# Optimization experiments

Hardware: AMD Instinct MI355X
Metric: run time of the kernel (lower is better)

The kernel has to match this reference:

```python
import jax, jax.numpy as jnp
import numpy as np

N = 100000      # nodes
E = 1600000     # edges (avg degree 16)
D = 64          # in_channels == conv widths == lin width
G = 64          # graphs in batch
OUT = 10        # out_channels


def setup_inputs() -> dict:
    key = jax.random.key(0)
    ks = jax.random.split(key, 20)
    s = 0.1
    inp = {
        "x": jax.random.normal(ks[0], (N, D), jnp.float32),
        "edge_index": jax.random.randint(ks[1], (2, E), 0, N, dtype=jnp.int64),
        "batch": jnp.sort(jax.random.randint(ks[2], (N,), 0, G, dtype=jnp.int64)),
    }
    k = 3
    for i in range(3):  # 3 SAGEConv layers: lin_l (Wl, bl) on aggregated, lin_r (Wr, no bias) on root
        inp[f"c{i}_Wl"] = jax.random.normal(ks[k], (D, D), jnp.float32) * s; k += 1
        inp[f"c{i}_bl"] = jnp.zeros((D,), jnp.float32)
        inp[f"c{i}_Wr"] = jax.random.normal(ks[k], (D, D), jnp.float32) * s; k += 1
    inp["l0_W"] = jax.random.normal(ks[k], (D, D), jnp.float32) * s; k += 1
    inp["l0_b"] = jnp.zeros((D,), jnp.float32)
    inp["out_W"] = jax.random.normal(ks[k], (D, OUT), jnp.float32) * s; k += 1
    inp["out_b"] = jnp.zeros((OUT,), jnp.float32)
    return inp


def reference(x, edge_index, batch,
              c0_Wl, c0_bl, c0_Wr,
              c1_Wl, c1_bl, c1_Wr,
              c2_Wl, c2_bl, c2_Wr,
              l0_W, l0_b, out_W, out_b):
    src, dst = edge_index[0], edge_index[1]
    # in-degree of each target node (mean conv aggregation), computed once
    deg = jax.ops.segment_sum(jnp.ones((E,), x.dtype), dst, num_segments=N)
    inv_deg = (1.0 / jnp.maximum(deg, 1.0))[:, None]

    def sage(h, Wl, bl, Wr):
        # gather source features, mean-aggregate at targets, then lin_l(agg) + lin_r(h)
        agg = jax.ops.segment_sum(h[src], dst, num_segments=N) * inv_deg
        return agg @ Wl + bl + h @ Wr

    h = jax.nn.relu(sage(x, c0_Wl, c0_bl, c0_Wr))
    h = jax.nn.relu(sage(h, c1_Wl, c1_bl, c1_Wr))
    h = jax.nn.relu(sage(h, c2_Wl, c2_bl, c2_Wr))

    # global mean pool over graphs
    cnt = jax.ops.segment_sum(jnp.ones((N,), h.dtype), batch, num_segments=G)
    g = jax.ops.segment_sum(h, batch, num_segments=G) / jnp.maximum(cnt, 1.0)[:, None]

    g = jax.nn.relu(g @ l0_W + l0_b)
    return g @ out_W + out_b  # [G, OUT]
```

## Files before the change

kernel.cpp:

```cpp
#include <hip/hip_runtime.h>
#include <hip/hip_fp16.h>

#define WPB 8
#define PADK 136
#define BSH 8
#define BNODES 256
#define SC_BLOCKS 256
#define HIST_BLOCKS 256
#define HSTRIDE 512

typedef _Float16 half8 __attribute__((ext_vector_type(8)));
typedef float floatx4 __attribute__((ext_vector_type(4)));

#define TS16(v) (((((v)[0] + (v)[1]) + ((v)[2] + (v)[3])) + (((v)[4] + (v)[5]) + ((v)[6] + (v)[7]))) + \
                 ((((v)[8] + (v)[9]) + ((v)[10] + (v)[11])) + (((v)[12] + (v)[13]) + ((v)[14] + (v)[15]))))

__global__ __launch_bounds__(256) void gnn_pre(const int* __restrict__ dst,
                                               int* __restrict__ bkt_cnt, int nbkt, int E,
                                               const int* __restrict__ batch,
                                               float* __restrict__ gcnt, int N,
                                               const float4* __restrict__ xin,
                                               ushort4* __restrict__ x16o, int n4,
                                               __half* __restrict__ x16,
                                               __half* __restrict__ hA,
                                               __half* __restrict__ hB,
                                               int* __restrict__ hist_all) {
    int tid = threadIdx.x;
    if (blockIdx.x < HIST_BLOCKS) {
        __shared__ int h[512];
        __shared__ int gb[64];
        for (int i = tid; i < nbkt; i += 256) h[i] = 0;
        if (tid < 64) gb[tid] = 0;
        __syncthreads();
        const int stride = HIST_BLOCKS * 256;
        for (int e = blockIdx.x * 256 + tid; e < E; e += stride)
            atomicAdd(&h[dst[e] >> BSH], 1);
        for (int i = blockIdx.x * 256 + tid; i < N; i += stride)
            atomicAdd(&gb[batch[i]], 1);
        __syncthreads();
        for (int i = tid; i < nbkt; i += 256) {
            int v = h[i];
            hist_all[blockIdx.x * HSTRIDE + i] = v;
            if (v) atomicAdd(&bkt_cnt[i], v);
        }
        if (tid < 64) {
            int v = gb[tid];
            if (v) atomicAdd(&gcnt[tid], (float)v);
        }
        if (blockIdx.x == 0 && tid < 64) {
            x16[(size_t)N * 64 + tid] = __ushort_as_half((unsigned short)0);
            hA[(size_t)N * 64 + tid] = __ushort_as_half((unsigned short)0);
            hB[(size_t)N * 64 + tid] = __ushort_as_half((unsigned short)0);
        }
    } else {
        int i = (blockIdx.x - HIST_BLOCKS) * 256 + tid;
        if (i < n4) {
            float4 f = xin[i];
            ushort4 o;
            o.x = __half_as_ushort(__float2half(f.x));
            o.y = __half_as_ushort(__float2half(f.y));
            o.z = __half_as_ushort(__float2half(f.z));
            o.w = __half_as_ushort(__float2half(f.w));
            x16o[i] = o;
        }
    }
}

__global__ void gnn_bkt_scan(const int* __restrict__ bkt_cnt, int* __restrict__ bkt_base,
                             int* __restrict__ row_ptr, int nbkt, int N) {
    int lane = threadIdx.x;
    int carry = 0;
    for (int base = 0; base < nbkt; base += 64) {
        int idx = base + lane;
        int v = (idx < nbkt) ? bkt_cnt[idx] : 0;
        int x = v;
#pragma unroll
        for (int off = 1; off < 64; off <<= 1) {
            int y = __shfl_up(x, off);
            if (lane >= off) x += y;
        }
        if (idx < nbkt) bkt_base[idx] = carry + (x - v);
        carry += __shfl(x, 63);
    }
    if (lane == 0) {
        bkt_base[nbkt] = carry;
        row_ptr[N] = carry;
    }
}

__global__ __launch_bounds__(256) void gnn_scan2(const int* __restrict__ hist_all,
                                                 const int* __restrict__ bkt_base,
                                                 int* __restrict__ blk_base_all, int nbkt) {
    int b = blockIdx.x;
    int t = threadIdx.x, lane = t & 63, wv = t >> 6;
    __shared__ int wsum[4];
    int v = hist_all[t * HSTRIDE + b];
    int x = v;
#pragma unroll
    for (int off = 1; off < 64; off <<= 1) {
        int y = __shfl_up(x, off);
        if (lane >= off) x += y;
    }
    if (lane == 63) wsum[wv] = x;
    __syncthreads();
    int wexcl = 0;
    for (int w = 0; w < wv; w++) wexcl += wsum[w];
    blk_base_all[t * HSTRIDE + b] = bkt_base[b] + wexcl + (x - v);
}

__global__ __launch_bounds__(256) void gnn_bkt_scatter(const int* __restrict__ src,
                                                       const int* __restrict__ dst,
                                                       const int* __restrict__ blk_base_all,
                                                       unsigned int* __restrict__ pairs,
                                                       int E, int nbkt) {
    __shared__ int cur[512];
    int tid = threadIdx.x;
    for (int i = tid; i < nbkt; i += 256) cur[i] = blk_base_all[blockIdx.x * HSTRIDE + i];
    __syncthreads();
    const int stride = SC_BLOCKS * 256;
    for (int e = blockIdx.x * 256 + tid; e < E; e += stride) {
        int d = dst[e];
        int b = d >> BSH;
        int p = atomicAdd(&cur[b], 1);
        pairs[p] = (unsigned int)src[e] | ((unsigned int)(d & (BNODES - 1)) << 24);
    }
}

__global__ __launch_bounds__(256) void gnn_bkt_csr(const unsigned int* __restrict__ pairs,
                                                   const int* __restrict__ bkt_base,
                                                   int* __restrict__ row_ptr,
                                                   float* __restrict__ inv_deg,
                                                   int* __restrict__ csr_src, int N) {
    __shared__ int hist[BNODES];
    __shared__ int excl[BNODES];
    __shared__ int cur[BNODES];
    int b = blockIdx.x;
    int base = bkt_base[b];
    int cnt = bkt_base[b + 1] - base;
    int nd0 = b << BSH;
    int tid = threadIdx.x;
    hist[tid] = 0;
    __syncthreads();
    for (int i = tid; i < cnt; i += 256) atomicAdd(&hist[pairs[base + i] >> 24], 1);
    __syncthreads();
    if (tid < 64) {
        int carry = 0;
#pragma unroll
        for (int c = 0; c < BNODES; c += 64) {
            int v = hist[c + tid];
            int x = v;
#pragma unroll
            for (int off = 1; off < 64; off <<= 1) {
                int y = __shfl_up(x, off);
                if (tid >= off) x += y;
            }
            excl[c + tid] = carry + (x - v);
            carry += __shfl(x, 63);
        }
    }
    __syncthreads();
    {
        int node = nd0 + tid;
        if (node < N) {
            row_ptr[node] = base + excl[tid];
            int d = hist[tid];
            inv_deg[node] = 1.0f / (float)(d > 1 ? d : 1);
        }
        cur[tid] = excl[tid];
    }
    __syncthreads();
    for (int i = tid; i < cnt; i += 256) {
        unsigned int u = pairs[base + i];
        int j = u >> 24;
        int pos = atomicAdd(&cur[j], 1);
        csr_src[base + pos] = (int)(u & 0xFFFFFFu);
    }
}

__global__ __launch_bounds__(512, 6) void gnn_sage(const __half* __restrict__ hin,
                                                   __half* __restrict__ hout,
                                                   const int* __restrict__ row_ptr,
                                                   const int* __restrict__ csr_src,
                                                   const float* __restrict__ inv_deg,
                                                   const float* __restrict__ Wl,
                                                   const float* __restrict__ bl,
                                                   const float* __restrict__ Wr, int n) {
    __shared__ _Float16 w_lds[64 * PADK];
    __shared__ _Float16 in_lds[WPB][16 * PADK];
    int tid = threadIdx.x, lane = tid & 63, wv = tid >> 6;
    for (int i = tid; i < 64 * 64; i += 512) {
        int k = i >> 6, nn = i & 63;
        w_lds[nn * PADK + k] = (_Float16)Wl[i];
        w_lds[nn * PADK + 64 + k] = (_Float16)Wr[i];
    }
    __syncthreads();
    int ngroups = (n + 15) >> 4;
    int g = blockIdx.x * WPB + wv;
    if (g >= ngroups) return;
    int m16 = lane & 15, quad = lane >> 4;
    float bias[4];
#pragma unroll
    for (int nt = 0; nt < 4; nt++) bias[nt] = bl[nt * 16 + m16];
    _Float16* my_in = in_lds[wv];
    const _Float16* hin16 = (const _Float16*)hin;
    int nd0 = g << 4;
    for (int j2 = 0; j2 < 16; j2 += 2) {
        int ndA = min(nd0 + j2, n - 1);
        int ndB = min(nd0 + j2 + 1, n - 1);
        int s0A = row_ptr[ndA], s1A = row_ptr[ndA + 1];
        int s0B = row_ptr[ndB], s1B = row_ptr[ndB + 1];
        float idgA = inv_deg[ndA], idgB = inv_deg[ndB];
        my_in[j2 * PADK + 64 + lane] = hin16[(size_t)ndA * 64 + lane];
        my_in[(j2 + 1) * PADK + 64 + lane] = hin16[(size_t)ndB * 64 + lane];
        float accA = 0.0f, accB = 0.0f;
        int cbA = min(64, s1A - s0A);
        int cbB = min(64, s1B - s0B);
        int eA = (lane < cbA) ? csr_src[s0A + lane] : n;
        int eB = (lane < cbB) ? csr_src[s0B + lane] : n;
#pragma unroll
        for (int ib = 0; ib < 4; ib++) {
            const int i0 = ib * 16;
            if (i0 < cbA) {
                float vA[16];
#pragma unroll
                for (int j = 0; j < 16; j++) {
                    int sj = __shfl(eA, i0 + j);
                    vA[j] = __half2float(hin[(size_t)sj * 64 + lane]);
                }
                accA += TS16(vA);
            }
            if (i0 < cbB) {
                float vB[16];
#pragma unroll
                for (int j = 0; j < 16; j++) {
                    int sj = __shfl(eB, i0 + j);
                    vB[j] = __half2float(hin[(size_t)sj * 64 + lane]);
                }
                accB += TS16(vB);
            }
        }
        for (int base = s0A + 64; base < s1A; base += 64) {
            int cb = min(64, s1A - base);
            int ei = (lane < cb) ? csr_src[base + lane] : n;
#pragma unroll
            for (int ib = 0; ib < 4; ib++) {
                const int i0 = ib * 16;
                if (i0 < cb) {
                    float v[16];
#pragma unroll
                    for (int j = 0; j < 16; j++) {
                        int s = __shfl(ei, i0 + j);
                        v[j] = __half2float(hin[(size_t)s * 64 + lane]);
                    }
                    accA += TS16(v);
                }
            }
        }
        for (int base = s0B + 64; base < s1B; base += 64) {
            int cb = min(64, s1B - base);
            int ei = (lane < cb) ? csr_src[base + lane] : n;
#pragma unroll
            for (int ib = 0; ib < 4; ib++) {
                const int i0 = ib * 16;
                if (i0 < cb) {
                    float v[16];
#pragma unroll
                    for (int j = 0; j < 16; j++) {
                        int s = __shfl(ei, i0 + j);
                        v[j] = __half2float(hin[(size_t)s * 64 + lane]);
                    }
                    accB += TS16(v);
                }
            }
        }
        my_in[j2 * PADK + lane] = (_Float16)(accA * idgA);
        my_in[(j2 + 1) * PADK + lane] = (_Float16)(accB * idgB);
    }
    half8 afrag[4];
    const _Float16* abase = my_in + m16 * PADK + quad * 8;
#pragma unroll
    for (int ks = 0; ks < 4; ks++) afrag[ks] = *(const half8*)(abase + ks * 32);
    floatx4 accv[4];
#pragma unroll
    for (int nt = 0; nt < 4; nt++) {
        accv[nt].x = 0.f; accv[nt].y = 0.f; accv[nt].z = 0.f; accv[nt].w = 0.f;
    }
#pragma unroll
    for (int nt = 0; nt < 4; nt++) {
        const _Float16* bbase = w_lds + (nt * 16 + m16) * PADK + quad * 8;
#pragma unroll
        for (int ks = 0; ks < 4; ks++) {
            half8 bfrag = *(const half8*)(bbase + ks * 32);
            accv[nt] = __builtin_amdgcn_mfma_f32_16x16x32_f16(afrag[ks], bfrag, accv[nt], 0, 0, 0);
        }
    }
#pragma unroll
    for (int nt = 0; nt < 4; nt++) {
#pragma unroll
        for (int r = 0; r < 4; r++) {
            int node = nd0 + quad * 4 + r;
            if (node < n) {
                float v = fmaxf(accv[nt][r] + bias[nt], 0.0f);
                hout[(size_t)node * 64 + nt * 16 + m16] = __float2half(v);
            }
        }
    }
}

__global__ __launch_bounds__(512, 6) void gnn_sage_pool(const __half* __restrict__ hin,
                                                        const int* __restrict__ row_ptr,
                                                        const int* __restrict__ csr_src,
                                                        const float* __restrict__ inv_deg,
                                                        const float* __restrict__ Wl,
                                                        const float* __restrict__ bl,
                                                        const float* __restrict__ Wr,
                                                        const int* __restrict__ batch,
                                                        float* __restrict__ gsum, int n) {
    __shared__ _Float16 w_lds[64 * PADK];
    __shared__ _Float16 in_lds[WPB][16 * PADK];
    int tid = threadIdx.x, lane = tid & 63, wv = tid >> 6;
    for (int i = tid; i < 64 * 64; i += 512) {
        int k = i >> 6, nn = i & 63;
        w_lds[nn * PADK + k] = (_Float16)Wl[i];
        w_lds[nn * PADK + 64 + k] = (_Float16)Wr[i];
    }
    __syncthreads();
    int ngroups = (n + 15) >> 4;
    int g = blockIdx.x * WPB + wv;
    if (g >= ngroups) return;
    int m16 = lane & 15, quad = lane >> 4;
    float bias[4];
#pragma unroll
    for (int nt = 0; nt < 4; nt++) bias[nt] = bl[nt * 16 + m16];
    _Float16* my_in = in_lds[wv];
    const _Float16* hin16 = (const _Float16*)hin;
    int nd0 = g << 4;
    for (int j2 = 0; j2 < 16; j2 += 2) {
        int ndA = min(nd0 + j2, n - 1);
        int ndB = min(nd0 + j2 + 1, n - 1);
        int s0A = row_ptr[ndA], s1A = row_ptr[ndA + 1];
        int s0B = row_ptr[ndB], s1B = row_ptr[ndB + 1];
        float idgA = inv_deg[ndA], idgB = inv_deg[ndB];
        my_in[j2 * PADK + 64 + lane] = hin16[(size_t)ndA * 64 + lane];
        my_in[(j2 + 1) * PADK + 64 + lane] = hin16[(size_t)ndB * 64 + lane];
        float accA = 0.0f, accB = 0.0f;
        int cbA = min(64, s1A - s0A);
        int cbB = min(64, s1B - s0B);
        int eA = (lane < cbA) ? csr_src[s0A + lane] : n;
        int eB = (lane < cbB) ? csr_src[s0B + lane] : n;
#pragma unroll
        for (int ib = 0; ib < 4; ib++) {
            const int i0 = ib * 16;
            if (i0 < cbA) {
                float vA[16];
#pragma unroll
                for (int j = 0; j < 16; j++) {
                    int sj = __shfl(eA, i0 + j);
                    vA[j] = __half2float(hin[(size_t)sj * 64 + lane]);
                }
                accA += TS16(vA);
            }
            if (i0 < cbB) {
                float vB[16];
#pragma unroll
                for (int j = 0; j < 16; j++) {
                    int sj = __shfl(eB, i0 + j);
                    vB[j] = __half2float(hin[(size_t)sj * 64 + lane]);
                }
                accB += TS16(vB);
            }
        }
        for (int base = s0A + 64; base < s1A; base += 64) {
            int cb = min(64, s1A - base);
            int ei = (lane < cb) ? csr_src[base + lane] : n;
#pragma unroll
            for (int ib = 0; ib < 4; ib++) {
                const int i0 = ib * 16;
                if (i0 < cb) {
                    float v[16];
#pragma unroll
                    for (int j = 0; j < 16; j++) {
                        int s = __shfl(ei, i0 + j);
                        v[j] = __half2float(hin[(size_t)s * 64 + lane]);
                    }
                    accA += TS16(v);
                }
            }
        }
        for (int base = s0B + 64; base < s1B; base += 64) {
            int cb = min(64, s1B - base);
            int ei = (lane < cb) ? csr_src[base + lane] : n;
#pragma unroll
            for (int ib = 0; ib < 4; ib++) {
                const int i0 = ib * 16;
                if (i0 < cb) {
                    float v[16];
#pragma unroll
                    for (int j = 0; j < 16; j++) {
                        int s = __shfl(ei, i0 + j);
                        v[j] = __half2float(hin[(size_t)s * 64 + lane]);
                    }
                    accB += TS16(v);
                }
            }
        }
        my_in[j2 * PADK + lane] = (_Float16)(accA * idgA);
        my_in[(j2 + 1) * PADK + lane] = (_Float16)(accB * idgB);
    }
    half8 afrag[4];
    const _Float16* abase = my_in + m16 * PADK + quad * 8;
#pragma unroll
    for (int ks = 0; ks < 4; ks++) afrag[ks] = *(const half8*)(abase + ks * 32);
    floatx4 accv[4];
#pragma unroll
    for (int nt = 0; nt < 4; nt++) {
        accv[nt].x = 0.f; accv[nt].y = 0.f; accv[nt].z = 0.f; accv[nt].w = 0.f;
    }
#pragma unroll
    for (int nt = 0; nt < 4; nt++) {
        const _Float16* bbase = w_lds + (nt * 16 + m16) * PADK + quad * 8;
#pragma unroll
        for (int ks = 0; ks < 4; ks++) {
            half8 bfrag = *(const half8*)(bbase + ks * 32);
            accv[nt] = __builtin_amdgcn_mfma_f32_16x16x32_f16(afrag[ks], bfrag, accv[nt], 0, 0, 0);
        }
    }
    int bFirst = batch[nd0];
    int bLast = batch[min(nd0 + 15, n - 1)];
    if (bFirst == bLast && nd0 + 15 < n) {
#pragma unroll
        for (int nt = 0; nt < 4; nt++) {
            float s = fmaxf(accv[nt][0] + bias[nt], 0.0f) + fmaxf(accv[nt][1] + bias[nt], 0.0f) +
                      fmaxf(accv[nt][2] + bias[nt], 0.0f) + fmaxf(accv[nt][3] + bias[nt], 0.0f);
            s += __shfl_xor(s, 16);
            s += __shfl_xor(s, 32);
            if (quad == 0) atomicAdd(&gsum[bFirst * 64 + nt * 16 + m16], s);
        }
    } else {
#pragma unroll
        for (int nt = 0; nt < 4; nt++) {
#pragma unroll
            for (int r = 0; r < 4; r++) {
                int node = nd0 + quad * 4 + r;
                if (node < n) {
                    int bg = batch[node];
                    float v = fmaxf(accv[nt][r] + bias[nt], 0.0f);
                    atomicAdd(&gsum[bg * 64 + nt * 16 + m16], v);
                }
            }
        }
    }
}

__global__ __launch_bounds__(256) void gnn_head(const float* __restrict__ gsum,
                                                const float* __restrict__ gcnt,
                                                const float* __restrict__ l0W,
                                                const float* __restrict__ l0b,
                                                const float* __restrict__ outW,
                                                const float* __restrict__ outb,
                                                float* __restrict__ out, int G, int OUT) {
    __shared__ float gm[64 * 64];
    __shared__ float t2[64 * 64];
    int tid = threadIdx.x;
    for (int i = tid; i < G * 64; i += 256) {
        int r = i >> 6;
        gm[i] = gsum[i] / fmaxf(gcnt[r], 1.0f);
    }
    __syncthreads();
    for (int i = tid; i < G * 64; i += 256) {
        int r = i >> 6, c = i & 63;
        float s = l0b[c];
#pragma unroll 8
        for (int k = 0; k < 64; k++) s += gm[(r << 6) + k] * l0W[(k << 6) + c];
        t2[i] = fmaxf(s, 0.0f);
    }
    __syncthreads();
    for (int i = tid; i < G * OUT; i += 256) {
        int r = i / OUT, c = i - r * OUT;
        float s = outb[c];
#pragma unroll 8
        for (int k = 0; k < 64; k++) s += t2[(r << 6) + k] * outW[k * OUT + c];
        out[i] = s;
    }
}

extern "C" void kernel_launch(void* const* d_in, const int* in_sizes, int n_in,
                              void* d_out, int out_size, void* d_ws, size_t ws_size,
                              hipStream_t stream) {
    const float* x = (const float*)d_in[0];
    const int* ei = (const int*)d_in[1];
    const int* batch = (const int*)d_in[2];
    const float* Wl[3] = {(const float*)d_in[3], (const float*)d_in[6], (const float*)d_in[9]};
    const float* bl[3] = {(const float*)d_in[4], (const float*)d_in[7], (const float*)d_in[10]};
    const float* Wr[3] = {(const float*)d_in[5], (const float*)d_in[8], (const float*)d_in[11]};
    const float* l0W = (const float*)d_in[12];
    const float* l0b = (const float*)d_in[13];
    const float* outW = (const float*)d_in[14];
    const float* outb = (const float*)d_in[15];

    int N = in_sizes[2];
    int E = in_sizes[1] / 2;
    int OUT = 10;
    int G = out_size / OUT;
    const int* src = ei;
    const int* dst = ei + E;
    int NBKT = (N + BNODES - 1) >> BSH;

    char* ws = (char*)d_ws;
    size_t off = 0;
    auto alloc = [&](size_t b) -> char* {
        char* p = ws + off;
        off = (off + b + 255) & ~(size_t)255;
        return p;
    };
    int* row_ptr = (int*)alloc((size_t)(N + 1) * 4);
    int* csr_src = (int*)alloc((size_t)E * 4);
    float* inv_deg = (float*)alloc((size_t)N * 4);
    size_t zoff = off;
    int* bkt_cnt = (int*)alloc((size_t)NBKT * 4);
    float* gcnt = (float*)alloc((size_t)G * 4);
    float* gsum = (float*)alloc((size_t)G * 64 * 4);
    size_t zlen = off - zoff;
    int* bkt_base = (int*)alloc((size_t)(NBKT + 1) * 4);
    int* hist_all = (int*)alloc((size_t)HIST_BLOCKS * HSTRIDE * 4);
    int* blk_base_all = (int*)alloc((size_t)HIST_BLOCKS * HSTRIDE * 4);
    unsigned int* pairs = (unsigned int*)alloc((size_t)E * 4);
    __half* x16 = (__half*)alloc((size_t)(N + 1) * 64 * 2);
    __half* hA = (__half*)alloc((size_t)(N + 1) * 64 * 2);
    __half* hB = (__half*)alloc((size_t)(N + 1) * 64 * 2);

    hipMemsetAsync(ws + zoff, 0, zlen, stream);

    int n4 = N * 64 / 4;
    int pre_blocks = HIST_BLOCKS + (n4 + 255) / 256;
    gnn_pre<<<pre_blocks, 256, 0, stream>>>(dst, bkt_cnt, NBKT, E, batch, gcnt, N,
                                            (const float4*)x, (ushort4*)x16, n4,
                                            x16, hA, hB, hist_all);
    gnn_bkt_scan<<<1, 64, 0, stream>>>(bkt_cnt, bkt_base, row_ptr, NBKT, N);
    gnn_scan2<<<NBKT, 256, 0, stream>>>(hist_all, bkt_base, blk_base_all, NBKT);
    gnn_bkt_scatter<<<SC_BLOCKS, 256, 0, stream>>>(src, dst, blk_base_all, pairs, E, NBKT);
    gnn_bkt_csr<<<NBKT, 256, 0, stream>>>(pairs, bkt_base, row_ptr, inv_deg, csr_src, N);

    int ngroups = (N + 15) >> 4;
    int sage_blocks = (ngroups + WPB - 1) / WPB;
    gnn_sage<<<sage_blocks, 512, 0, stream>>>(x16, hA, row_ptr, csr_src, inv_deg,
                                              Wl[0], bl[0], Wr[0], N);
    gnn_sage<<<sage_blocks, 512, 0, stream>>>(hA, hB, row_ptr, csr_src, inv_deg,
                                              Wl[1], bl[1], Wr[1], N);
    gnn_sage_pool<<<sage_blocks, 512, 0, stream>>>(hB, row_ptr, csr_src, inv_deg,
                                                   Wl[2], bl[2], Wr[2], batch, gsum, N);

    gnn_head<<<1, 256, 0, stream>>>(gsum, gcnt, l0W, l0b, outW, outb, (float*)d_out, G, OUT);
}
```

Before: 345.8 us.

## Gather two neighbors per wave with half2 loads and prefetch CSR indices

The gather loop in both SAGE kernels now has each half-wave read a different neighbor row as 32-bit half2 words, so each wave load instruction covers two edges. Partial sums from the two halves are combined with a cross-half shuffle. Row pointers, inverse degrees and the first 64 edge indices for all 16 nodes are loaded up front and passed around with shuffles instead of being reloaded per node pair. The extra registers force occupancy from 6 down to 4 waves-per-SIMD in the launch bounds, which may reduce latency hiding for this gather-bound kernel.

```diff
diff --git a/kernel.cpp b/kernel.cpp
--- a/kernel.cpp
+++ b/kernel.cpp
@@ -10,10 +10,9 @@
 #define HSTRIDE 512
 
 typedef _Float16 half8 __attribute__((ext_vector_type(8)));
+typedef _Float16 half2v __attribute__((ext_vector_type(2)));
 typedef float floatx4 __attribute__((ext_vector_type(4)));
-
-#define TS16(v) (((((v)[0] + (v)[1]) + ((v)[2] + (v)[3])) + (((v)[4] + (v)[5]) + ((v)[6] + (v)[7]))) + \
-                 ((((v)[8] + (v)[9]) + ((v)[10] + (v)[11])) + (((v)[12] + (v)[13]) + ((v)[14] + (v)[15]))))
+typedef float floatx2 __attribute__((ext_vector_type(2)));
 
 __global__ __launch_bounds__(256) void gnn_pre(const int* __restrict__ dst,
                                                int* __restrict__ bkt_cnt, int nbkt, int E,
@@ -177,7 +176,21 @@
     }
 }
 
-__global__ __launch_bounds__(512, 6) void gnn_sage(const __half* __restrict__ hin,
+#define GATH16(eReg, ibase, accum)                                          \
+    {                                                                       \
+        floatx2 v[8];                                                       \
+        _Pragma("unroll") for (int j = 0; j < 8; j++) {                     \
+            int sj = __shfl(eReg, (ibase) + 2 * j + hf);                    \
+            half2v hh = hin2v[(size_t)sj * 32 + col];                       \
+            floatx2 f;                                                      \
+            f.x = (float)hh[0];                                             \
+            f.y = (float)hh[1];                                             \
+            v[j] = f;                                                       \
+        }                                                                   \
+        accum += ((v[0] + v[1]) + (v[2] + v[3])) + ((v[4] + v[5]) + (v[6] + v[7])); \
+    }
+
+__global__ __launch_bounds__(512, 4) void gnn_sage(const __half* __restrict__ hin,
                                                    __half* __restrict__ hout,
                                                    const int* __restrict__ row_ptr,
                                                    const int* __restrict__ csr_src,
@@ -198,83 +211,77 @@
     int g = blockIdx.x * WPB + wv;
     if (g >= ngroups) return;
     int m16 = lane & 15, quad = lane >> 4;
+    int hf = lane >> 5, col = lane & 31;
     float bias[4];
 #pragma unroll
     for (int nt = 0; nt < 4; nt++) bias[nt] = bl[nt * 16 + m16];
     _Float16* my_in = in_lds[wv];
-    const _Float16* hin16 = (const _Float16*)hin;
+    const unsigned* hin32 = (const unsigned*)hin;
+    const half2v* hin2v = (const half2v*)hin;
     int nd0 = g << 4;
-    for (int j2 = 0; j2 < 16; j2 += 2) {
-        int ndA = min(nd0 + j2, n - 1);
-        int ndB = min(nd0 + j2 + 1, n - 1);
-        int s0A = row_ptr[ndA], s1A = row_ptr[ndA + 1];
-        int s0B = row_ptr[ndB], s1B = row_ptr[ndB + 1];
-        float idgA = inv_deg[ndA], idgB = inv_deg[ndB];
-        my_in[j2 * PADK + 64 + lane] = hin16[(size_t)ndA * 64 + lane];
-        my_in[(j2 + 1) * PADK + 64 + lane] = hin16[(size_t)ndB * 64 + lane];
-        float accA = 0.0f, accB = 0.0f;
-        int cbA = min(64, s1A - s0A);
-        int cbB = min(64, s1B - s0B);
-        int eA = (lane < cbA) ? csr_src[s0A + lane] : n;
-        int eB = (lane < cbB) ? csr_src[s0B + lane] : n;
+    int nclamp = n - 1 - nd0;
+    int idx = nd0 + lane;
+    int rr = (lane <= 16) ? row_ptr[min(idx, n)] : 0;
+    float ig = (lane < 16) ? inv_deg[min(idx, n - 1)] : 0.0f;
+
+#pragma unroll
+    for (int jp = 0; jp < 8; jp++) {
+        int j2 = jp << 1;
+        int nd = nd0 + min(j2 + hf, nclamp);
+        unsigned u = hin32[(size_t)nd * 32 + col];
+        ((unsigned*)(my_in + (j2 + hf) * PADK + 64))[col] = u;
+    }
+
+    int ef[16];
+#pragma unroll
+    for (int j = 0; j < 16; j++) {
+        int jj = min(j, nclamp);
+        int s0 = __shfl(rr, jj), s1 = __shfl(rr, jj + 1);
+        int cb = min(64, s1 - s0);
+        ef[j] = (lane < cb) ? csr_src[s0 + lane] : n;
+    }
+
+#pragma unroll
+    for (int jp = 0; jp < 8; jp++) {
+        int j2 = jp << 1;
+        int jjA = min(j2, nclamp), jjB = min(j2 + 1, nclamp);
+        int s0A = __shfl(rr, jjA), s1A = __shfl(rr, jjA + 1);
+        int s0B = __shfl(rr, jjB), s1B = __shfl(rr, jjB + 1);
+        float idgA = __shfl(ig, jjA), idgB = __shfl(ig, jjB);
+        int cbA = min(64, s1A - s0A), cbB = min(64, s1B - s0B);
+        floatx2 accA, accB;
+        accA.x = 0.f; accA.y = 0.f;
+        accB.x = 0.f; accB.y = 0.f;
 #pragma unroll
         for (int ib = 0; ib < 4; ib++) {
-            const int i0 = ib * 16;
-            if (i0 < cbA) {
-                float vA[16];
-#pragma unroll
-                for (int j = 0; j < 16; j++) {
-                    int sj = __shfl(eA, i0 + j);
-                    vA[j] = __half2float(hin[(size_t)sj * 64 + lane]);
-                }
-                accA += TS16(vA);
-            }
-            if (i0 < cbB) {
-                float vB[16];
-#pragma unroll
-                for (int j = 0; j < 16; j++) {
-                    int sj = __shfl(eB, i0 + j);
-                    vB[j] = __half2float(hin[(size_t)sj * 64 + lane]);
-                }
-                accB += TS16(vB);
-            }
+            if (ib * 16 < cbA) GATH16(ef[j2], ib * 16, accA);
+            if (ib * 16 < cbB) GATH16(ef[j2 + 1], ib * 16, accB);
         }
         for (int base = s0A + 64; base < s1A; base += 64) {
             int cb = min(64, s1A - base);
             int ei = (lane < cb) ? csr_src[base + lane] : n;
 #pragma unroll
-            for (int ib = 0; ib < 4; ib++) {
-                const int i0 = ib * 16;
-                if (i0 < cb) {
-                    float v[16];
-#pragma unroll
-                    for (int j = 0; j < 16; j++) {
-                        int s = __shfl(ei, i0 + j);
-                        v[j] = __half2float(hin[(size_t)s * 64 + lane]);
-                    }
-                    accA += TS16(v);
-                }
-            }
+            for (int ib = 0; ib < 4; ib++)
+                if (ib * 16 < cb) GATH16(ei, ib * 16, accA);
         }
         for (int base = s0B + 64; base < s1B; base += 64) {
             int cb = min(64, s1B - base);
             int ei = (lane < cb) ? csr_src[base + lane] : n;
 #pragma unroll
-            for (int ib = 0; ib < 4; ib++) {
-                const int i0 = ib * 16;
-                if (i0 < cb) {
-                    float v[16];
-#pragma unroll
-                    for (int j = 0; j < 16; j++) {
-                        int s = __shfl(ei, i0 + j);
-                        v[j] = __half2float(hin[(size_t)s * 64 + lane]);
-                    }
-                    accB += TS16(v);
-                }
-            }
-        }
-        my_in[j2 * PADK + lane] = (_Float16)(accA * idgA);
-        my_in[(j2 + 1) * PADK + lane] = (_Float16)(accB * idgB);
+            for (int ib = 0; ib < 4; ib++)
+                if (ib * 16 < cb) GATH16(ei, ib * 16, accB);
+        }
+        accA.x += __shfl_xor(accA.x, 32);
+        accA.y += __shfl_xor(accA.y, 32);
+        accB.x += __shfl_xor(accB.x, 32);
+        accB.y += __shfl_xor(accB.y, 32);
+        floatx2 wv2;
+        wv2.x = hf ? accB.x * idgB : accA.x * idgA;
+        wv2.y = hf ? accB.y * idgB : accA.y * idgA;
+        __half2 hw;
+        hw.x = __float2half(wv2.x);
+        hw.y = __float2half(wv2.y);
+        ((__half2*)(my_in + (j2 + hf) * PADK))[col] = hw;
     }
     half8 afrag[4];
     const _Float16* abase = my_in + m16 * PADK + quad * 8;
@@ -307,7 +314,7 @@
     }
 }
 
-__global__ __launch_bounds__(512, 6) void gnn_sage_pool(const __half* __restrict__ hin,
+__global__ __launch_bounds__(512, 4) void gnn_sage_pool(const __half* __restrict__ hin,
                                                         const int* __restrict__ row_ptr,
                                                         const int* __restrict__ csr_src,
                                                         const float* __restrict__ inv_deg,
@@ -329,83 +336,77 @@
     int g = blockIdx.x * WPB + wv;
     if (g >= ngroups) return;
     int m16 = lane & 15, quad = lane >> 4;
+    int hf = lane >> 5, col = lane & 31;
     float bias[4];
 #pragma unroll
     for (int nt = 0; nt < 4; nt++) bias[nt] = bl[nt * 16 + m16];
     _Float16* my_in = in_lds[wv];
-    const _Float16* hin16 = (const _Float16*)hin;
+    const unsigned* hin32 = (const unsigned*)hin;
+    const half2v* hin2v = (const half2v*)hin;
     int nd0 = g << 4;
-    for (int j2 = 0; j2 < 16; j2 += 2) {
-        int ndA = min(nd0 + j2, n - 1);
-        int ndB = min(nd0 + j2 + 1, n - 1);
-        int s0A = row_ptr[ndA], s1A = row_ptr[ndA + 1];
-        int s0B = row_ptr[ndB], s1B = row_ptr[ndB + 1];
-        float idgA = inv_deg[ndA], idgB = inv_deg[ndB];
-        my_in[j2 * PADK + 64 + lane] = hin16[(size_t)ndA * 64 + lane];
-        my_in[(j2 + 1) * PADK + 64 + lane] = hin16[(size_t)ndB * 64 + lane];
-        float accA = 0.0f, accB = 0.0f;
-        int cbA = min(64, s1A - s0A);
-        int cbB = min(64, s1B - s0B);
-        int eA = (lane < cbA) ? csr_src[s0A + lane] : n;
-        int eB = (lane < cbB) ? csr_src[s0B + lane] : n;
+    int nclamp = n - 1 - nd0;
+    int idx = nd0 + lane;
+    int rr = (lane <= 16) ? row_ptr[min(idx, n)] : 0;
+    float ig = (lane < 16) ? inv_deg[min(idx, n - 1)] : 0.0f;
+
+#pragma unroll
+    for (int jp = 0; jp < 8; jp++) {
+        int j2 = jp << 1;
+        int nd = nd0 + min(j2 + hf, nclamp);
+        unsigned u = hin32[(size_t)nd * 32 + col];
+        ((unsigned*)(my_in + (j2 + hf) * PADK + 64))[col] = u;
+    }
+
+    int ef[16];
+#pragma unroll
+    for (int j = 0; j < 16; j++) {
+        int jj = min(j, nclamp);
+        int s0 = __shfl(rr, jj), s1 = __shfl(rr, jj + 1);
+        int cb = min(64, s1 - s0);
+        ef[j] = (lane < cb) ? csr_src[s0 + lane] : n;
+    }
+
+#pragma unroll
+    for (int jp = 0; jp < 8; jp++) {
+        int j2 = jp << 1;
+        int jjA = min(j2, nclamp), jjB = min(j2 + 1, nclamp);
+        int s0A = __shfl(rr, jjA), s1A = __shfl(rr, jjA + 1);
+        int s0B = __shfl(rr, jjB), s1B = __shfl(rr, jjB + 1);
+        float idgA = __shfl(ig, jjA), idgB = __shfl(ig, jjB);
+        int cbA = min(64, s1A - s0A), cbB = min(64, s1B - s0B);
+        floatx2 accA, accB;
+        accA.x = 0.f; accA.y = 0.f;
+        accB.x = 0.f; accB.y = 0.f;
 #pragma unroll
         for (int ib = 0; ib < 4; ib++) {
-            const int i0 = ib * 16;
-            if (i0 < cbA) {
-                float vA[16];
-#pragma unroll
-                for (int j = 0; j < 16; j++) {
-                    int sj = __shfl(eA, i0 + j);
-                    vA[j] = __half2float(hin[(size_t)sj * 64 + lane]);
-                }
-                accA += TS16(vA);
-            }
-            if (i0 < cbB) {
-                float vB[16];
-#pragma unroll
-                for (int j = 0; j < 16; j++) {
-                    int sj = __shfl(eB, i0 + j);
-                    vB[j] = __half2float(hin[(size_t)sj * 64 + lane]);
-                }
-                accB += TS16(vB);
-            }
+            if (ib * 16 < cbA) GATH16(ef[j2], ib * 16, accA);
+            if (ib * 16 < cbB) GATH16(ef[j2 + 1], ib * 16, accB);
         }
         for (int base = s0A + 64; base < s1A; base += 64) {
             int cb = min(64, s1A - base);
             int ei = (lane < cb) ? csr_src[base + lane] : n;
 #pragma unroll
-            for (int ib = 0; ib < 4; ib++) {
-                const int i0 = ib * 16;
-                if (i0 < cb) {
-                    float v[16];
-#pragma unroll
-                    for (int j = 0; j < 16; j++) {
-                        int s = __shfl(ei, i0 + j);
-                        v[j] = __half2float(hin[(size_t)s * 64 + lane]);
-                    }
-                    accA += TS16(v);
-                }
-            }
+            for (int ib = 0; ib < 4; ib++)
+                if (ib * 16 < cb) GATH16(ei, ib * 16, accA);
         }
         for (int base = s0B + 64; base < s1B; base += 64) {
             int cb = min(64, s1B - base);
             int ei = (lane < cb) ? csr_src[base + lane] : n;
 #pragma unroll
-            for (int ib = 0; ib < 4; ib++) {
-                const int i0 = ib * 16;
-                if (i0 < cb) {
-                    float v[16];
-#pragma unroll
-                    for (int j = 0; j < 16; j++) {
-                        int s = __shfl(ei, i0 + j);
-                        v[j] = __half2float(hin[(size_t)s * 64 + lane]);
-                    }
-                    accB += TS16(v);
-                }
-            }
-        }
-        my_in[j2 * PADK + lane] = (_Float16)(accA * idgA);
-        my_in[(j2 + 1) * PADK + lane] = (_Float16)(accB * idgB);
+            for (int ib = 0; ib < 4; ib++)
+                if (ib * 16 < cb) GATH16(ei, ib * 16, accB);
+        }
+        accA.x += __shfl_xor(accA.x, 32);
+        accA.y += __shfl_xor(accA.y, 32);
+        accB.x += __shfl_xor(accB.x, 32);
+        accB.y += __shfl_xor(accB.y, 32);
+        floatx2 wv2;
+        wv2.x = hf ? accB.x * idgB : accA.x * idgA;
+        wv2.y = hf ? accB.y * idgB : accA.y * idgA;
+        __half2 hw;
+        hw.x = __float2half(wv2.x);
+        hw.y = __float2half(wv2.y);
+        ((__half2*)(my_in + (j2 + hf) * PADK))[col] = hw;
     }
     half8 afrag[4];
     const _Float16* abase = my_in + m16 * PADK + quad * 8;
```

New measurement: 324.4 us. -6.2%, faster.
